# Kernel tuning notes

Measured on AMD Instinct MI355X. Metric: run time of the kernel, lower is better.

The kernel has to match this reference:

```python
import jax, jax.numpy as jnp
import numpy as np

N_NODES = 10000
N_EDGES = 160000
N_IN, H, HEADS, HOUT = 128, 256, 2, 256
BATCH_SIZE = 8192


def setup_inputs() -> dict:
    key = jax.random.key(0)
    ks = jax.random.split(key, 20)
    s = 0.05
    inp = {
        "x": jax.random.normal(ks[0], (N_NODES, N_IN), dtype=jnp.float32),
        "edge_index": jax.random.randint(ks[1], (2, N_EDGES), 0, N_NODES, dtype=jnp.int64),
        "batch_size": BATCH_SIZE,
        # encoder: Linear(128,256), LayerNorm(256), ReLU, Linear(256,256)
        "enc_w1": jax.random.normal(ks[2], (H, N_IN), dtype=jnp.float32) * s,
        "enc_b1": jnp.zeros((H,), jnp.float32),
        "ln_g": jnp.ones((H,), jnp.float32),
        "ln_b": jnp.zeros((H,), jnp.float32),
        "enc_w2": jax.random.normal(ks[3], (H, H), dtype=jnp.float32) * s,
        "enc_b2": jnp.zeros((H,), jnp.float32),
        # GATConv(256, 256, heads=2): lin 256->512 (no bias), att vectors, out bias [512]
        "gat_w": jax.random.normal(ks[4], (HEADS * HOUT, H), dtype=jnp.float32) * s,
        "att_src": jax.random.normal(ks[5], (HEADS, HOUT), dtype=jnp.float32) * s,
        "att_dst": jax.random.normal(ks[6], (HEADS, HOUT), dtype=jnp.float32) * s,
        "gat_bias": jnp.zeros((HEADS * HOUT,), jnp.float32),
        # skip: Linear(256, 512)
        "skip_w": jax.random.normal(ks[7], (HEADS * HOUT, H), dtype=jnp.float32) * s,
        "skip_b": jnp.zeros((HEADS * HOUT,), jnp.float32),
        # decoder: Linear(512,1024) -> LeakyReLU(0.1) -> Linear(1024,1)
        "dec_w1": jax.random.normal(ks[8], (4 * H, HEADS * HOUT), dtype=jnp.float32) * s,
        "dec_b1": jnp.zeros((4 * H,), jnp.float32),
        "dec_w2": jax.random.normal(ks[9], (1, 4 * H), dtype=jnp.float32) * s,
        "dec_b2": jnp.zeros((1,), jnp.float32),
    }
    return inp


def _elu(x, alpha):
    return jnp.where(x > 0, x, alpha * (jnp.exp(x) - 1.0))


def _leaky(x, slope):
    return jnp.where(x > 0, x, slope * x)


def _forward(x, edge_index, batch_size, enc_w1, enc_b1, ln_g, ln_b, enc_w2, enc_b2,
             gat_w, att_src, att_dst, gat_bias, skip_w, skip_b,
             dec_w1, dec_b1, dec_w2, dec_b2):
    n = x.shape[0]
    # encoder
    h = x @ enc_w1.T + enc_b1
    mu = jnp.mean(h, axis=-1, keepdims=True)
    var = jnp.mean((h - mu) ** 2, axis=-1, keepdims=True)
    h = (h - mu) * jax.lax.rsqrt(var + 1e-5) * ln_g + ln_b
    h = jax.nn.relu(h)
    h = h @ enc_w2.T + enc_b2  # [N, 256]

    # GATConv with self-loops (PyG default add_self_loops=True)
    loops = jnp.arange(n, dtype=edge_index.dtype)
    src = jnp.concatenate([edge_index[0], loops])
    tgt = jnp.concatenate([edge_index[1], loops])

    xs = (h @ gat_w.T).reshape(n, HEADS, HOUT)  # [N, heads, out]
    a_src = jnp.sum(xs * att_src[None], axis=-1)  # [N, heads]
    a_dst = jnp.sum(xs * att_dst[None], axis=-1)  # [N, heads]

    e = _leaky(a_src[src] + a_dst[tgt], 0.2)  # [E', heads]
    m = jax.ops.segment_max(e, tgt, num_segments=n)
    w = jnp.exp(e - m[tgt])
    z = jax.ops.segment_sum(w, tgt, num_segments=n)
    alpha = w / z[tgt]  # [E', heads]

    msg = xs[src] * alpha[:, :, None]  # [E', heads, out]
    agg = jax.ops.segment_sum(msg, tgt, num_segments=n).reshape(n, HEADS * HOUT)
    conv = agg + gat_bias

    out = conv + h @ skip_w.T + skip_b
    out = _elu(out, 0.1)  # ELU(alpha=0.1)

    # decoder
    d = _leaky(out @ dec_w1.T + dec_b1, 0.1)
    y = d @ dec_w2.T + dec_b2
    return y[:batch_size]


def reference(x, edge_index, batch_size, enc_w1, enc_b1, ln_g, ln_b, enc_w2, enc_b2,
              gat_w, att_src, att_dst, gat_bias, skip_w, skip_b,
              dec_w1, dec_b1, dec_w2, dec_b2):
    return _forward(x, edge_index, batch_size, enc_w1, enc_b1, ln_g, ln_b, enc_w2, enc_b2,
                    gat_w, att_src, att_dst, gat_bias, skip_w, skip_b,
                    dec_w1, dec_b1, dec_w2, dec_b2)
```

## Files before the change

### kernel.cpp

```cpp
#include <hip/hip_runtime.h>


#define N_NODES  10000
#define N_EDGES  160000
#define E_TOT    (N_EDGES + N_NODES)
#define NBATCH   8192
#define DIM_IN   128
#define DIM_H    256
#define DIM_GAT  512
#define DIM_DEC  1024
#define MPAD     10112

typedef short bf16x8 __attribute__((ext_vector_type(8)));
typedef float f32x4  __attribute__((ext_vector_type(4)));

__device__ __forceinline__ ushort f2bf(float f) {
    union { float f; unsigned u; } c; c.f = f;
    unsigned u = c.u + 0x7FFFu + ((c.u >> 16) & 1u);
    return (ushort)(u >> 16);
}
__device__ __forceinline__ float bf2f(ushort h) {
    union { unsigned u; float f; } c; c.u = ((unsigned)h) << 16; return c.f;
}

template<int BM, int BN, int BK, int TM, int TN>
__global__ __launch_bounds__(256)
void gemm_kernel(const float* __restrict__ A, const float* __restrict__ W,
                 const float* __restrict__ bias, float* __restrict__ C,
                 int M, int N, int K)
{
    constexpr int TX = BN / TN;
    constexpr int TY = BM / TM;
    static_assert(TX * TY == 256, "block must be 256 threads");
    __shared__ float As[BK][BM + 4];
    __shared__ float Ws[BK][BN + 4];

    const int tid = threadIdx.x;
    const int tx  = tid % TX;
    const int ty  = tid / TX;
    const int bm  = blockIdx.x * BM;
    const int bn  = blockIdx.y * BN;

    float acc[TM][TN];
    #pragma unroll
    for (int i = 0; i < TM; ++i)
        #pragma unroll
        for (int j = 0; j < TN; ++j) acc[i][j] = 0.f;

    constexpr int A_LOADS = BM * BK / 4 / 256;
    constexpr int W_LOADS = BN * BK / 4 / 256;
    constexpr int KQ = BK / 4;

    for (int k0 = 0; k0 < K; k0 += BK) {
        #pragma unroll
        for (int l = 0; l < A_LOADS; ++l) {
            int idx = tid + l * 256, row = idx / KQ, kq = idx % KQ;
            int grow = bm + row;
            float4 v = make_float4(0.f, 0.f, 0.f, 0.f);
            if (grow < M)
                v = *reinterpret_cast<const float4*>(&A[(size_t)grow * K + k0 + kq * 4]);
            As[kq * 4 + 0][row] = v.x; As[kq * 4 + 1][row] = v.y;
            As[kq * 4 + 2][row] = v.z; As[kq * 4 + 3][row] = v.w;
        }
        #pragma unroll
        for (int l = 0; l < W_LOADS; ++l) {
            int idx = tid + l * 256, row = idx / KQ, kq = idx % KQ;
            float4 v = *reinterpret_cast<const float4*>(&W[(size_t)(bn + row) * K + k0 + kq * 4]);
            Ws[kq * 4 + 0][row] = v.x; Ws[kq * 4 + 1][row] = v.y;
            Ws[kq * 4 + 2][row] = v.z; Ws[kq * 4 + 3][row] = v.w;
        }
        __syncthreads();
        #pragma unroll
        for (int kk = 0; kk < BK; ++kk) {
            float af[TM], wf[TN];
            #pragma unroll
            for (int i = 0; i < TM; ++i) af[i] = As[kk][ty * TM + i];
            #pragma unroll
            for (int j = 0; j < TN; ++j) wf[j] = Ws[kk][tx * TN + j];
            #pragma unroll
            for (int i = 0; i < TM; ++i)
                #pragma unroll
                for (int j = 0; j < TN; ++j)
                    acc[i][j] = fmaf(af[i], wf[j], acc[i][j]);
        }
        __syncthreads();
    }

    #pragma unroll
    for (int i = 0; i < TM; ++i) {
        int grow = bm + ty * TM + i;
        if (grow < M) {
            #pragma unroll
            for (int j = 0; j < TN; ++j) {
                int gcol = bn + tx * TN + j;
                C[(size_t)grow * N + gcol] = acc[i][j] + bias[gcol];
            }
        }
    }
}

__device__ __forceinline__ void stage_tile(ushort* T, const ushort* __restrict__ G,
                                           int rowbase, int K, int k0, int tid, int wv)
{
    #pragma unroll
    for (int i = 0; i < 4; ++i) {
        int m   = i * 32 + (tid >> 3);
        int scb = ((tid & 7) << 4) ^ ((m & 7) << 4);
        const char* gsrc = (const char*)G + ((size_t)(rowbase + m) * K + k0) * 2 + scb;
        char* ldst = (char*)T + i * 4096 + wv * 1024;
        __builtin_amdgcn_global_load_lds(
            (const __attribute__((address_space(1))) void*)gsrc,
            (__attribute__((address_space(3))) void*)ldst, 16, 0, 0);
    }
}

__device__ __forceinline__ bf16x8 ldfrag(const ushort* T, int row, int kcb)
{
    int addr = (row << 7) + (kcb ^ ((row & 7) << 4));
    return *reinterpret_cast<const bf16x8*>(reinterpret_cast<const char*>(T) + addr);
}

template<int EPI>
__global__ __launch_bounds__(256, 2)
void mgemm(const ushort* __restrict__ Ah, const ushort* __restrict__ Al,
           const ushort* __restrict__ Wh, const ushort* __restrict__ Wl,
           const float* __restrict__ bias, const float* __restrict__ bias2,
           const float* __restrict__ addmat, float* __restrict__ outF,
           ushort* __restrict__ outHi, ushort* __restrict__ outLo,
           const float* __restrict__ w2, const float* __restrict__ b2,
           float* __restrict__ aS, float* __restrict__ aD,
           float* __restrict__ yout, int M, int N, int K)
{
    __shared__ __align__(16) ushort tAh[8192];
    __shared__ __align__(16) ushort tAl[8192];
    __shared__ __align__(16) ushort tWh[8192];
    __shared__ __align__(16) ushort tWl[8192];

    const int tid    = threadIdx.x;
    const int lane   = tid & 63;
    const int wv     = tid >> 6;
    const int wr     = wv >> 1, wc = wv & 1;
    const int bm     = blockIdx.x * 128;
    const int bn     = blockIdx.y * 128;
    const int lane15 = lane & 15;
    const int kgrp16 = (lane >> 4) << 4;
    const int r0     = (lane >> 4) << 2;

    f32x4 acc[4][4];
    const f32x4 zero = {0.f, 0.f, 0.f, 0.f};
    #pragma unroll
    for (int i = 0; i < 4; ++i)
        #pragma unroll
        for (int j = 0; j < 4; ++j) acc[i][j] = zero;

    for (int k0 = 0; k0 < K; k0 += 64) {
        stage_tile(tAh, Ah, bm, K, k0, tid, wv);
        stage_tile(tAl, Al, bm, K, k0, tid, wv);
        stage_tile(tWh, Wh, bn, K, k0, tid, wv);
        stage_tile(tWl, Wl, bn, K, k0, tid, wv);
        __syncthreads();
        #pragma unroll
        for (int kk = 0; kk < 2; ++kk) {
            const int kcb = kk * 64 + kgrp16;
            bf16x8 ah[4], al[4], wh[4], wl[4];
            #pragma unroll
            for (int f = 0; f < 4; ++f) {
                ah[f] = ldfrag(tAh, wr * 64 + f * 16 + lane15, kcb);
                al[f] = ldfrag(tAl, wr * 64 + f * 16 + lane15, kcb);
                wh[f] = ldfrag(tWh, wc * 64 + f * 16 + lane15, kcb);
                wl[f] = ldfrag(tWl, wc * 64 + f * 16 + lane15, kcb);
            }
            #pragma unroll
            for (int fm = 0; fm < 4; ++fm)
                #pragma unroll
                for (int fn = 0; fn < 4; ++fn) {
                    acc[fm][fn] = __builtin_amdgcn_mfma_f32_16x16x32_bf16(ah[fm], wh[fn], acc[fm][fn], 0, 0, 0);
                    acc[fm][fn] = __builtin_amdgcn_mfma_f32_16x16x32_bf16(ah[fm], wl[fn], acc[fm][fn], 0, 0, 0);
                    acc[fm][fn] = __builtin_amdgcn_mfma_f32_16x16x32_bf16(al[fm], wh[fn], acc[fm][fn], 0, 0, 0);
                }
        }
        __syncthreads();
    }

    if (EPI == 0) {
        const int head = bn >> 8;
        #pragma unroll
        for (int fm = 0; fm < 4; ++fm) {
            #pragma unroll
            for (int r = 0; r < 4; ++r) {
                int row = bm + wr * 64 + fm * 16 + r0 + r;
                if (row < M) {
                    float sp = 0.f, dp = 0.f;
                    #pragma unroll
                    for (int fn = 0; fn < 4; ++fn) {
                        int col = bn + wc * 64 + fn * 16 + lane15;
                        float v = acc[fm][fn][r];
                        outHi[(size_t)row * N + col] = f2bf(v);
                        sp = fmaf(v, bias[col], sp);
                        dp = fmaf(v, bias2[col], dp);
                    }
                    sp += __shfl_xor(sp, 1); sp += __shfl_xor(sp, 2);
                    sp += __shfl_xor(sp, 4); sp += __shfl_xor(sp, 8);
                    dp += __shfl_xor(dp, 1); dp += __shfl_xor(dp, 2);
                    dp += __shfl_xor(dp, 4); dp += __shfl_xor(dp, 8);
                    if (lane15 == 0) {
                        atomicAdd(&aS[row * 2 + head], sp);
                        atomicAdd(&aD[row * 2 + head], dp);
                    }
                }
            }
        }
    } else if (EPI == 1 || EPI == 2) {
        #pragma unroll
        for (int fm = 0; fm < 4; ++fm) {
            #pragma unroll
            for (int r = 0; r < 4; ++r) {
                int row = bm + wr * 64 + fm * 16 + r0 + r;
                if (row < M) {
                    #pragma unroll
                    for (int fn = 0; fn < 4; ++fn) {
                        int col = bn + wc * 64 + fn * 16 + lane15;
                        float v = acc[fm][fn][r] + bias[col];
                        if (EPI == 2) {
                            v += bias2[col] + addmat[(size_t)row * N + col];
                            v = v > 0.f ? v : 0.1f * (expf(v) - 1.f);
                        }
                        ushort h = f2bf(v);
                        outHi[(size_t)row * N + col] = h;
                        outLo[(size_t)row * N + col] = f2bf(v - bf2f(h));
                    }
                }
            }
        }
    } else {
        #pragma unroll
        for (int fm = 0; fm < 4; ++fm) {
            #pragma unroll
            for (int r = 0; r < 4; ++r) {
                int row = bm + wr * 64 + fm * 16 + r0 + r;
                float part = 0.f;
                #pragma unroll
                for (int fn = 0; fn < 4; ++fn) {
                    int col = bn + wc * 64 + fn * 16 + lane15;
                    float v = acc[fm][fn][r] + bias[col];
                    v = v > 0.f ? v : 0.1f * v;
                    part = fmaf(v, w2[col], part);
                }
                part += __shfl_xor(part, 1);
                part += __shfl_xor(part, 2);
                part += __shfl_xor(part, 4);
                part += __shfl_xor(part, 8);
                if (lane15 == 0 && row < M) {
                    float add = part + ((blockIdx.y == 0 && wc == 0) ? b2[0] : 0.f);
                    atomicAdd(&yout[row], add);
                }
            }
        }
    }
}

__global__ __launch_bounds__(256)
void split_kernel(const float* __restrict__ src, ushort* __restrict__ hi,
                  ushort* __restrict__ lo, int n)
{
    int i = blockIdx.x * 256 + threadIdx.x;
    if (i < n) {
        float v = src[i];
        ushort h = f2bf(v);
        hi[i] = h;
        lo[i] = f2bf(v - bf2f(h));
    }
}

__global__ void detect_kernel(const int* __restrict__ ei32, int* __restrict__ eflag)
{
    if (blockIdx.x == 0 && threadIdx.x == 0) {
        int s = 0;
        #pragma unroll
        for (int i = 0; i < 64; ++i) s |= ei32[2 * i + 1];
        eflag[0] = (s == 0) ? 2 : 1;
    }
}

__global__ __launch_bounds__(256)
void ln_relu_split_kernel(const float* __restrict__ h1, const float* __restrict__ g,
                          const float* __restrict__ b, ushort* __restrict__ hi,
                          ushort* __restrict__ lo)
{
    int wave = threadIdx.x >> 6, lane = threadIdx.x & 63;
    int row = blockIdx.x * 4 + wave;
    if (row >= N_NODES) return;
    float4 v = *reinterpret_cast<const float4*>(&h1[(size_t)row * DIM_H + lane * 4]);
    float s  = v.x + v.y + v.z + v.w;
    float sq = v.x * v.x + v.y * v.y + v.z * v.z + v.w * v.w;
    #pragma unroll
    for (int m = 1; m <= 32; m <<= 1) { s += __shfl_xor(s, m); sq += __shfl_xor(sq, m); }
    float mu  = s * (1.0f / 256.0f);
    float var = sq * (1.0f / 256.0f) - mu * mu;
    float rs  = 1.0f / sqrtf(var + 1e-5f);
    float4 gg = *reinterpret_cast<const float4*>(&g[lane * 4]);
    float4 bb = *reinterpret_cast<const float4*>(&b[lane * 4]);
    float o[4];
    o[0] = fmaxf((v.x - mu) * rs * gg.x + bb.x, 0.f);
    o[1] = fmaxf((v.y - mu) * rs * gg.y + bb.y, 0.f);
    o[2] = fmaxf((v.z - mu) * rs * gg.z + bb.z, 0.f);
    o[3] = fmaxf((v.w - mu) * rs * gg.w + bb.w, 0.f);
    ushort4 vh, vl;
    ushort* ph = &vh.x; ushort* pl = &vl.x;
    #pragma unroll
    for (int q = 0; q < 4; ++q) {
        ushort hh = f2bf(o[q]);
        ph[q] = hh;
        pl[q] = f2bf(o[q] - bf2f(hh));
    }
    *reinterpret_cast<ushort4*>(&hi[(size_t)row * DIM_H + lane * 4]) = vh;
    *reinterpret_cast<ushort4*>(&lo[(size_t)row * DIM_H + lane * 4]) = vl;
}

__global__ __launch_bounds__(256)
void edge_w_kernel(const int* __restrict__ ei, const int* __restrict__ eflag,
                   const float* __restrict__ asrc, const float* __restrict__ adst,
                   float* __restrict__ wbuf, float* __restrict__ zbuf,
                   int* __restrict__ counts)
{
    int e = blockIdx.x * 256 + threadIdx.x;
    if (e >= E_TOT) return;
    const int stride = eflag[0];
    int src, tgt;
    if (e < N_EDGES) {
        src = ei[(size_t)stride * e];
        tgt = ei[(size_t)stride * (N_EDGES + e)];
    } else {
        src = tgt = e - N_EDGES;
    }
    #pragma unroll
    for (int hh = 0; hh < 2; ++hh) {
        float v = asrc[src * 2 + hh] + adst[tgt * 2 + hh];
        v = v > 0.f ? v : 0.2f * v;
        float w = expf(v);
        wbuf[e * 2 + hh] = w;
        atomicAdd(&zbuf[tgt * 2 + hh], w);
    }
    atomicAdd(&counts[tgt], 1);
}

__global__ __launch_bounds__(1024)
void scan_kernel(const int* __restrict__ counts, int* __restrict__ rowst)
{
    __shared__ int part[1024];
    const int t = threadIdx.x;
    const int base = t * 10;
    int loc[10];
    int s = 0;
    #pragma unroll
    for (int i = 0; i < 10; ++i) {
        int idx = base + i;
        int v = (idx < N_NODES) ? counts[idx] : 0;
        loc[i] = s;
        s += v;
    }
    part[t] = s;
    __syncthreads();
    for (int off = 1; off < 1024; off <<= 1) {
        int v = (t >= off) ? part[t - off] : 0;
        __syncthreads();
        part[t] += v;
        __syncthreads();
    }
    int chunk_excl = part[t] - s;
    #pragma unroll
    for (int i = 0; i < 10; ++i) {
        int idx = base + i;
        if (idx <= N_NODES) rowst[idx] = chunk_excl + loc[i];
    }
}

__global__ __launch_bounds__(256)
void scatter_kernel(const int* __restrict__ ei, const int* __restrict__ eflag,
                    const int* __restrict__ rowst,
                    int* __restrict__ cursor, unsigned int* __restrict__ ebuf)
{
    int e = blockIdx.x * 256 + threadIdx.x;
    if (e >= E_TOT) return;
    const int stride = eflag[0];
    int src, tgt;
    if (e < N_EDGES) {
        src = ei[(size_t)stride * e];
        tgt = ei[(size_t)stride * (N_EDGES + e)];
    } else {
        src = tgt = e - N_EDGES;
    }
    int pos = atomicAdd(&cursor[tgt], 1);
    ebuf[rowst[tgt] + pos] = ((unsigned int)e << 14) | (unsigned int)src;
}

__global__ __launch_bounds__(256)
void agg_kernel(const ushort* __restrict__ xs_b,
                const float* __restrict__ wbuf, const float* __restrict__ zbuf,
                const int* __restrict__ rowst, const unsigned int* __restrict__ ebuf,
                float* __restrict__ agg)
{
    const int n = blockIdx.x;
    const int t = threadIdx.x;
    const int h = t >> 7;
    const float inv = 1.0f / zbuf[n * 2 + h];
    float acc0 = 0.f, acc1 = 0.f;
    const int beg = rowst[n], end = rowst[n + 1];
    int j = beg;
    for (; j + 3 < end; j += 4) {
        unsigned pk0 = ebuf[j],     pk1 = ebuf[j + 1];
        unsigned pk2 = ebuf[j + 2], pk3 = ebuf[j + 3];
        float w0 = wbuf[(pk0 >> 14) * 2 + h];
        float w1 = wbuf[(pk1 >> 14) * 2 + h];
        float w2 = wbuf[(pk2 >> 14) * 2 + h];
        float w3 = wbuf[(pk3 >> 14) * 2 + h];
        ushort2 x0 = *reinterpret_cast<const ushort2*>(&xs_b[(size_t)(pk0 & 0x3FFFu) * DIM_GAT + 2 * t]);
        ushort2 x1 = *reinterpret_cast<const ushort2*>(&xs_b[(size_t)(pk1 & 0x3FFFu) * DIM_GAT + 2 * t]);
        ushort2 x2 = *reinterpret_cast<const ushort2*>(&xs_b[(size_t)(pk2 & 0x3FFFu) * DIM_GAT + 2 * t]);
        ushort2 x3 = *reinterpret_cast<const ushort2*>(&xs_b[(size_t)(pk3 & 0x3FFFu) * DIM_GAT + 2 * t]);
        float a0 = w0 * inv, a1 = w1 * inv, a2 = w2 * inv, a3 = w3 * inv;
        acc0 = fmaf(bf2f(x0.x), a0, acc0); acc1 = fmaf(bf2f(x0.y), a0, acc1);
        acc0 = fmaf(bf2f(x1.x), a1, acc0); acc1 = fmaf(bf2f(x1.y), a1, acc1);
        acc0 = fmaf(bf2f(x2.x), a2, acc0); acc1 = fmaf(bf2f(x2.y), a2, acc1);
        acc0 = fmaf(bf2f(x3.x), a3, acc0); acc1 = fmaf(bf2f(x3.y), a3, acc1);
    }
    for (; j < end; ++j) {
        unsigned pk = ebuf[j];
        float w = wbuf[(pk >> 14) * 2 + h];
        ushort2 x = *reinterpret_cast<const ushort2*>(&xs_b[(size_t)(pk & 0x3FFFu) * DIM_GAT + 2 * t]);
        float a = w * inv;
        acc0 = fmaf(bf2f(x.x), a, acc0);
        acc1 = fmaf(bf2f(x.y), a, acc1);
    }
    agg[(size_t)n * DIM_GAT + 2 * t]     = acc0;
    agg[(size_t)n * DIM_GAT + 2 * t + 1] = acc1;
}

extern "C" void kernel_launch(void* const* d_in, const int* in_sizes, int n_in,
                              void* d_out, int out_size, void* d_ws, size_t ws_size,
                              hipStream_t stream)
{
    const float* x        = (const float*)d_in[0];
    const int*   ei       = (const int*)  d_in[1];
    const float* enc_w1   = (const float*)d_in[3];
    const float* enc_b1   = (const float*)d_in[4];
    const float* ln_g     = (const float*)d_in[5];
    const float* ln_b     = (const float*)d_in[6];
    const float* enc_w2   = (const float*)d_in[7];
    const float* enc_b2   = (const float*)d_in[8];
    const float* gat_w    = (const float*)d_in[9];
    const float* att_src  = (const float*)d_in[10];
    const float* att_dst  = (const float*)d_in[11];
    const float* gat_bias = (const float*)d_in[12];
    const float* skip_w   = (const float*)d_in[13];
    const float* skip_b   = (const float*)d_in[14];
    const float* dec_w1   = (const float*)d_in[15];
    const float* dec_b1   = (const float*)d_in[16];
    const float* dec_w2   = (const float*)d_in[17];
    const float* dec_b2   = (const float*)d_in[18];
    float* y = (float*)d_out;

    float* ws = (float*)d_ws;
    float*  h1      = ws;
    ushort* h1ln_hi = (ushort*)(ws + 2560000);
    ushort* h1ln_lo = h1ln_hi + (size_t)MPAD * DIM_H;
    ushort* xs_b    = (ushort*)ws;
    ushort* outb_hi = (ushort*)ws;
    ushort* outb_lo = outb_hi + (size_t)NBATCH * DIM_GAT;
    ushort* h_hi = (ushort*)(ws + 5242880);
    ushort* h_lo = h_hi + (size_t)MPAD * DIM_H;
    float* agg = ws + 7842880;
    ushort* wsp = (ushort*)(ws + 12037184);
    ushort* w2h = wsp;
    ushort* w2l = w2h + 65536;
    ushort* gwh = w2l + 65536;
    ushort* gwl = gwh + 131072;
    ushort* swh = gwl + 131072;
    ushort* swl = swh + 131072;
    ushort* d1h = swl + 131072;
    ushort* d1l = d1h + 524288;
    float* S      = ws + 12889152;
    float* asrc   = S;
    float* adst   = S + 20000;
    float* zbuf   = S + 40000;
    int*   counts = (int*)(S + 60000);
    int*   cursor = counts + 10000;
    float* wbuf   = S + 80000;
    int*   rowst  = (int*)(S + 420000);
    unsigned int* ebuf = (unsigned int*)(rowst + 10001);
    int*   eflag  = (int*)(ebuf + 170000);

    hipMemsetAsync(asrc, 0, 80000 * sizeof(float), stream);
    hipMemsetAsync(y, 0, (size_t)NBATCH * sizeof(float), stream);
    detect_kernel<<<1, 1, 0, stream>>>(ei, eflag);

    split_kernel<<<256,  256, 0, stream>>>(enc_w2, w2h, w2l, 65536);
    split_kernel<<<512,  256, 0, stream>>>(gat_w,  gwh, gwl, 131072);
    split_kernel<<<512,  256, 0, stream>>>(skip_w, swh, swl, 131072);
    split_kernel<<<2048, 256, 0, stream>>>(dec_w1, d1h, d1l, 524288);

    gemm_kernel<64, 64, 16, 4, 4><<<dim3(157, 4), 256, 0, stream>>>(
        x, enc_w1, enc_b1, h1, N_NODES, DIM_H, DIM_IN);
    ln_relu_split_kernel<<<2500, 256, 0, stream>>>(h1, ln_g, ln_b, h1ln_hi, h1ln_lo);
    mgemm<1><<<dim3(79, 2), 256, 0, stream>>>(
        h1ln_hi, h1ln_lo, w2h, w2l, enc_b2, nullptr, nullptr,
        nullptr, h_hi, h_lo, nullptr, nullptr, nullptr, nullptr, nullptr,
        N_NODES, DIM_H, DIM_H);
    mgemm<0><<<dim3(79, 4), 256, 0, stream>>>(
        h_hi, h_lo, gwh, gwl, att_src, att_dst, nullptr,
        nullptr, xs_b, nullptr, nullptr, nullptr, asrc, adst, nullptr,
        N_NODES, DIM_GAT, DIM_H);
    edge_w_kernel<<<(E_TOT + 255) / 256, 256, 0, stream>>>(
        ei, eflag, asrc, adst, wbuf, zbuf, counts);
    scan_kernel<<<1, 1024, 0, stream>>>(counts, rowst);
    scatter_kernel<<<(E_TOT + 255) / 256, 256, 0, stream>>>(
        ei, eflag, rowst, cursor, ebuf);
    agg_kernel<<<NBATCH, 256, 0, stream>>>(xs_b, wbuf, zbuf, rowst, ebuf, agg);
    mgemm<2><<<dim3(64, 4), 256, 0, stream>>>(
        h_hi, h_lo, swh, swl, skip_b, gat_bias, agg,
        nullptr, outb_hi, outb_lo, nullptr, nullptr, nullptr, nullptr, nullptr,
        NBATCH, DIM_GAT, DIM_H);
    mgemm<3><<<dim3(64, 8), 256, 0, stream>>>(
        outb_hi, outb_lo, d1h, d1l, dec_b1, nullptr, nullptr,
        nullptr, nullptr, nullptr, dec_w2, dec_b2, nullptr, nullptr, y,
        NBATCH, DIM_DEC, DIM_GAT);
}
```

Baseline: 275.7 us.

## Fuse encoder GEMM with LayerNorm, merge prep kernels, drop decoder lo-split

The first encoder linear layer now computes full 256-wide rows per block, and LayerNorm, ReLU and the bf16 hi/lo split are done in its epilogue. This removes the fp32 h1 round trip and one launch. The four weight-split kernels and the edge-format detect kernel are merged into one prep launch. The decoder GEMM now uses only the hi part of its activation input, cutting one of three MFMAs per step plus the lo staging and stores, at some cost in accuracy.

Measured after the change: 284.9 us. 3.3% more time.

```diff
diff --git a/kernel.cpp b/kernel.cpp
--- a/kernel.cpp
+++ b/kernel.cpp
@@ -23,15 +23,14 @@
     union { unsigned u; float f; } c; c.u = ((unsigned)h) << 16; return c.f;
 }
 
-template<int BM, int BN, int BK, int TM, int TN>
 __global__ __launch_bounds__(256)
-void gemm_kernel(const float* __restrict__ A, const float* __restrict__ W,
-                 const float* __restrict__ bias, float* __restrict__ C,
-                 int M, int N, int K)
-{
-    constexpr int TX = BN / TN;
-    constexpr int TY = BM / TM;
-    static_assert(TX * TY == 256, "block must be 256 threads");
+void enc1_ln_kernel(const float* __restrict__ A, const float* __restrict__ W,
+                    const float* __restrict__ bias,
+                    const float* __restrict__ g, const float* __restrict__ b,
+                    ushort* __restrict__ hi, ushort* __restrict__ lo)
+{
+    constexpr int BM = 64, BN = 256, BK = 16, TM = 8, TN = 8, TX = 32;
+    constexpr int KQ = BK / 4;
     __shared__ float As[BK][BM + 4];
     __shared__ float Ws[BK][BN + 4];
 
@@ -39,7 +38,6 @@
     const int tx  = tid % TX;
     const int ty  = tid / TX;
     const int bm  = blockIdx.x * BM;
-    const int bn  = blockIdx.y * BN;
 
     float acc[TM][TN];
     #pragma unroll
@@ -47,25 +45,20 @@
         #pragma unroll
         for (int j = 0; j < TN; ++j) acc[i][j] = 0.f;
 
-    constexpr int A_LOADS = BM * BK / 4 / 256;
-    constexpr int W_LOADS = BN * BK / 4 / 256;
-    constexpr int KQ = BK / 4;
-
-    for (int k0 = 0; k0 < K; k0 += BK) {
-        #pragma unroll
-        for (int l = 0; l < A_LOADS; ++l) {
-            int idx = tid + l * 256, row = idx / KQ, kq = idx % KQ;
+    for (int k0 = 0; k0 < DIM_IN; k0 += BK) {
+        {
+            int row = tid / KQ, kq = tid % KQ;
             int grow = bm + row;
             float4 v = make_float4(0.f, 0.f, 0.f, 0.f);
-            if (grow < M)
-                v = *reinterpret_cast<const float4*>(&A[(size_t)grow * K + k0 + kq * 4]);
+            if (grow < N_NODES)
+                v = *reinterpret_cast<const float4*>(&A[(size_t)grow * DIM_IN + k0 + kq * 4]);
             As[kq * 4 + 0][row] = v.x; As[kq * 4 + 1][row] = v.y;
             As[kq * 4 + 2][row] = v.z; As[kq * 4 + 3][row] = v.w;
         }
         #pragma unroll
-        for (int l = 0; l < W_LOADS; ++l) {
+        for (int l = 0; l < 4; ++l) {
             int idx = tid + l * 256, row = idx / KQ, kq = idx % KQ;
-            float4 v = *reinterpret_cast<const float4*>(&W[(size_t)(bn + row) * K + k0 + kq * 4]);
+            float4 v = *reinterpret_cast<const float4*>(&W[(size_t)row * DIM_IN + k0 + kq * 4]);
             Ws[kq * 4 + 0][row] = v.x; Ws[kq * 4 + 1][row] = v.y;
             Ws[kq * 4 + 2][row] = v.z; Ws[kq * 4 + 3][row] = v.w;
         }
@@ -89,12 +82,33 @@
     #pragma unroll
     for (int i = 0; i < TM; ++i) {
         int grow = bm + ty * TM + i;
-        if (grow < M) {
+        float vals[TN];
+        float s = 0.f, sq = 0.f;
+        #pragma unroll
+        for (int j = 0; j < TN; ++j) {
+            float v = acc[i][j] + bias[tx * TN + j];
+            vals[j] = v; s += v; sq += v * v;
+        }
+        #pragma unroll
+        for (int m = 1; m <= 16; m <<= 1) { s += __shfl_xor(s, m); sq += __shfl_xor(sq, m); }
+        float mu  = s * (1.0f / 256.0f);
+        float var = sq * (1.0f / 256.0f) - mu * mu;
+        float rs  = 1.0f / sqrtf(var + 1e-5f);
+        if (grow < N_NODES) {
+            ushort4 vh[2], vl[2];
+            ushort* ph = (ushort*)vh; ushort* pl = (ushort*)vl;
             #pragma unroll
             for (int j = 0; j < TN; ++j) {
-                int gcol = bn + tx * TN + j;
-                C[(size_t)grow * N + gcol] = acc[i][j] + bias[gcol];
+                int col = tx * TN + j;
+                float o = fmaxf((vals[j] - mu) * rs * g[col] + b[col], 0.f);
+                ushort hh = f2bf(o);
+                ph[j] = hh;
+                pl[j] = f2bf(o - bf2f(hh));
             }
+            *reinterpret_cast<ushort4*>(&hi[(size_t)grow * DIM_H + tx * TN])     = vh[0];
+            *reinterpret_cast<ushort4*>(&hi[(size_t)grow * DIM_H + tx * TN + 4]) = vh[1];
+            *reinterpret_cast<ushort4*>(&lo[(size_t)grow * DIM_H + tx * TN])     = vl[0];
+            *reinterpret_cast<ushort4*>(&lo[(size_t)grow * DIM_H + tx * TN + 4]) = vl[1];
         }
     }
 }
@@ -155,7 +169,7 @@
 
     for (int k0 = 0; k0 < K; k0 += 64) {
         stage_tile(tAh, Ah, bm, K, k0, tid, wv);
-        stage_tile(tAl, Al, bm, K, k0, tid, wv);
+        if (EPI != 3) stage_tile(tAl, Al, bm, K, k0, tid, wv);
         stage_tile(tWh, Wh, bn, K, k0, tid, wv);
         stage_tile(tWl, Wl, bn, K, k0, tid, wv);
         __syncthreads();
@@ -166,7 +180,7 @@
             #pragma unroll
             for (int f = 0; f < 4; ++f) {
                 ah[f] = ldfrag(tAh, wr * 64 + f * 16 + lane15, kcb);
-                al[f] = ldfrag(tAl, wr * 64 + f * 16 + lane15, kcb);
+                if (EPI != 3) al[f] = ldfrag(tAl, wr * 64 + f * 16 + lane15, kcb);
                 wh[f] = ldfrag(tWh, wc * 64 + f * 16 + lane15, kcb);
                 wl[f] = ldfrag(tWl, wc * 64 + f * 16 + lane15, kcb);
             }
@@ -176,7 +190,8 @@
                 for (int fn = 0; fn < 4; ++fn) {
                     acc[fm][fn] = __builtin_amdgcn_mfma_f32_16x16x32_bf16(ah[fm], wh[fn], acc[fm][fn], 0, 0, 0);
                     acc[fm][fn] = __builtin_amdgcn_mfma_f32_16x16x32_bf16(ah[fm], wl[fn], acc[fm][fn], 0, 0, 0);
-                    acc[fm][fn] = __builtin_amdgcn_mfma_f32_16x16x32_bf16(al[fm], wh[fn], acc[fm][fn], 0, 0, 0);
+                    if (EPI != 3)
+                        acc[fm][fn] = __builtin_amdgcn_mfma_f32_16x16x32_bf16(al[fm], wh[fn], acc[fm][fn], 0, 0, 0);
                 }
         }
         __syncthreads();
@@ -227,7 +242,7 @@
                         }
                         ushort h = f2bf(v);
                         outHi[(size_t)row * N + col] = h;
-                        outLo[(size_t)row * N + col] = f2bf(v - bf2f(h));
+                        if (outLo) outLo[(size_t)row * N + col] = f2bf(v - bf2f(h));
                     }
                 }
             }
@@ -260,61 +275,29 @@
 }
 
 __global__ __launch_bounds__(256)
-void split_kernel(const float* __restrict__ src, ushort* __restrict__ hi,
-                  ushort* __restrict__ lo, int n)
+void prep_kernel(const int* __restrict__ ei32, int* __restrict__ eflag,
+                 const float* __restrict__ s0, ushort* __restrict__ h0, ushort* __restrict__ l0,
+                 const float* __restrict__ s1, ushort* __restrict__ h1p, ushort* __restrict__ l1,
+                 const float* __restrict__ s2, ushort* __restrict__ h2, ushort* __restrict__ l2,
+                 const float* __restrict__ s3, ushort* __restrict__ h3, ushort* __restrict__ l3)
 {
     int i = blockIdx.x * 256 + threadIdx.x;
-    if (i < n) {
-        float v = src[i];
-        ushort h = f2bf(v);
-        hi[i] = h;
-        lo[i] = f2bf(v - bf2f(h));
-    }
-}
-
-__global__ void detect_kernel(const int* __restrict__ ei32, int* __restrict__ eflag)
-{
-    if (blockIdx.x == 0 && threadIdx.x == 0) {
+    if (i == 0) {
         int s = 0;
         #pragma unroll
-        for (int i = 0; i < 64; ++i) s |= ei32[2 * i + 1];
+        for (int q = 0; q < 64; ++q) s |= ei32[2 * q + 1];
         eflag[0] = (s == 0) ? 2 : 1;
     }
-}
-
-__global__ __launch_bounds__(256)
-void ln_relu_split_kernel(const float* __restrict__ h1, const float* __restrict__ g,
-                          const float* __restrict__ b, ushort* __restrict__ hi,
-                          ushort* __restrict__ lo)
-{
-    int wave = threadIdx.x >> 6, lane = threadIdx.x & 63;
-    int row = blockIdx.x * 4 + wave;
-    if (row >= N_NODES) return;
-    float4 v = *reinterpret_cast<const float4*>(&h1[(size_t)row * DIM_H + lane * 4]);
-    float s  = v.x + v.y + v.z + v.w;
-    float sq = v.x * v.x + v.y * v.y + v.z * v.z + v.w * v.w;
-    #pragma unroll
-    for (int m = 1; m <= 32; m <<= 1) { s += __shfl_xor(s, m); sq += __shfl_xor(sq, m); }
-    float mu  = s * (1.0f / 256.0f);
-    float var = sq * (1.0f / 256.0f) - mu * mu;
-    float rs  = 1.0f / sqrtf(var + 1e-5f);
-    float4 gg = *reinterpret_cast<const float4*>(&g[lane * 4]);
-    float4 bb = *reinterpret_cast<const float4*>(&b[lane * 4]);
-    float o[4];
-    o[0] = fmaxf((v.x - mu) * rs * gg.x + bb.x, 0.f);
-    o[1] = fmaxf((v.y - mu) * rs * gg.y + bb.y, 0.f);
-    o[2] = fmaxf((v.z - mu) * rs * gg.z + bb.z, 0.f);
-    o[3] = fmaxf((v.w - mu) * rs * gg.w + bb.w, 0.f);
-    ushort4 vh, vl;
-    ushort* ph = &vh.x; ushort* pl = &vl.x;
-    #pragma unroll
-    for (int q = 0; q < 4; ++q) {
-        ushort hh = f2bf(o[q]);
-        ph[q] = hh;
-        pl[q] = f2bf(o[q] - bf2f(hh));
-    }
-    *reinterpret_cast<ushort4*>(&hi[(size_t)row * DIM_H + lane * 4]) = vh;
-    *reinterpret_cast<ushort4*>(&lo[(size_t)row * DIM_H + lane * 4]) = vl;
+    const float* s; ushort* ph; ushort* pl; int off;
+    if      (i < 65536)  { s = s0; ph = h0;  pl = l0; off = i; }
+    else if (i < 196608) { s = s1; ph = h1p; pl = l1; off = i - 65536; }
+    else if (i < 327680) { s = s2; ph = h2;  pl = l2; off = i - 196608; }
+    else if (i < 851968) { s = s3; ph = h3;  pl = l3; off = i - 327680; }
+    else return;
+    float v = s[off];
+    ushort hh = f2bf(v);
+    ph[off] = hh;
+    pl[off] = f2bf(v - bf2f(hh));
 }
 
 __global__ __launch_bounds__(256)
@@ -461,12 +444,10 @@
     float* y = (float*)d_out;
 
     float* ws = (float*)d_ws;
-    float*  h1      = ws;
     ushort* h1ln_hi = (ushort*)(ws + 2560000);
     ushort* h1ln_lo = h1ln_hi + (size_t)MPAD * DIM_H;
     ushort* xs_b    = (ushort*)ws;
     ushort* outb_hi = (ushort*)ws;
-    ushort* outb_lo = outb_hi + (size_t)NBATCH * DIM_GAT;
     ushort* h_hi = (ushort*)(ws + 5242880);
     ushort* h_lo = h_hi + (size_t)MPAD * DIM_H;
     float* agg = ws + 7842880;
@@ -492,16 +473,14 @@
 
     hipMemsetAsync(asrc, 0, 80000 * sizeof(float), stream);
     hipMemsetAsync(y, 0, (size_t)NBATCH * sizeof(float), stream);
-    detect_kernel<<<1, 1, 0, stream>>>(ei, eflag);
-
-    split_kernel<<<256,  256, 0, stream>>>(enc_w2, w2h, w2l, 65536);
-    split_kernel<<<512,  256, 0, stream>>>(gat_w,  gwh, gwl, 131072);
-    split_kernel<<<512,  256, 0, stream>>>(skip_w, swh, swl, 131072);
-    split_kernel<<<2048, 256, 0, stream>>>(dec_w1, d1h, d1l, 524288);
-
-    gemm_kernel<64, 64, 16, 4, 4><<<dim3(157, 4), 256, 0, stream>>>(
-        x, enc_w1, enc_b1, h1, N_NODES, DIM_H, DIM_IN);
-    ln_relu_split_kernel<<<2500, 256, 0, stream>>>(h1, ln_g, ln_b, h1ln_hi, h1ln_lo);
+
+    prep_kernel<<<3328, 256, 0, stream>>>(
+        ei, eflag,
+        enc_w2, w2h, w2l, gat_w, gwh, gwl,
+        skip_w, swh, swl, dec_w1, d1h, d1l);
+
+    enc1_ln_kernel<<<157, 256, 0, stream>>>(
+        x, enc_w1, enc_b1, ln_g, ln_b, h1ln_hi, h1ln_lo);
     mgemm<1><<<dim3(79, 2), 256, 0, stream>>>(
         h1ln_hi, h1ln_lo, w2h, w2l, enc_b2, nullptr, nullptr,
         nullptr, h_hi, h_lo, nullptr, nullptr, nullptr, nullptr, nullptr,
@@ -518,10 +497,10 @@
     agg_kernel<<<NBATCH, 256, 0, stream>>>(xs_b, wbuf, zbuf, rowst, ebuf, agg);
     mgemm<2><<<dim3(64, 4), 256, 0, stream>>>(
         h_hi, h_lo, swh, swl, skip_b, gat_bias, agg,
-        nullptr, outb_hi, outb_lo, nullptr, nullptr, nullptr, nullptr, nullptr,
+        nullptr, outb_hi, nullptr, nullptr, nullptr, nullptr, nullptr, nullptr,
         NBATCH, DIM_GAT, DIM_H);
     mgemm<3><<<dim3(64, 8), 256, 0, stream>>>(
-        outb_hi, outb_lo, d1h, d1l, dec_b1, nullptr, nullptr,
+        outb_hi, nullptr, d1h, d1l, dec_b1, nullptr, nullptr,
         nullptr, nullptr, nullptr, dec_w2, dec_b2, nullptr, nullptr, y,
         NBATCH, DIM_DEC, DIM_GAT);
 }
```
